# Performance work log

Hardware: AMD Instinct MI355X
Metric: run time of the kernel (lower is better)

## Reference

```python
import jax, jax.numpy as jnp
import numpy as np

EPS = 1e-5

def layer_norm(x, g, b):
    mu = jnp.mean(x, axis=-1, keepdims=True)
    var = jnp.mean(jnp.square(x - mu), axis=-1, keepdims=True)
    return (x - mu) * jax.lax.rsqrt(var + EPS) * g + b

def setup_inputs() -> dict:
    key = jax.random.key(0)
    ks = jax.random.split(key, 8)
    B, T, D, H = 8, 2048, 32, 4
    hd = D // H
    s = 0.05
    return {
        "x": jax.random.normal(ks[0], (B, T, D), jnp.float32),
        "Wq": jax.random.normal(ks[1], (H, D, hd), jnp.float32) * s,
        "Wk": jax.random.normal(ks[2], (H, D, hd), jnp.float32) * s,
        "Wv": jax.random.normal(ks[3], (H, D, hd), jnp.float32) * s,
        "Wproj": jax.random.normal(ks[4], (D, D), jnp.float32) * s,
        "bproj": jnp.zeros((D,), jnp.float32),
        "ln1_g": jnp.ones((D,), jnp.float32),
        "ln1_b": jnp.zeros((D,), jnp.float32),
        "W1": jax.random.normal(ks[5], (D, 4 * D), jnp.float32) * s,
        "b1": jnp.zeros((4 * D,), jnp.float32),
        "W2": jax.random.normal(ks[6], (4 * D, D), jnp.float32) * s,
        "b2": jnp.zeros((D,), jnp.float32),
        "ln2_g": jnp.ones((D,), jnp.float32),
        "ln2_b": jnp.zeros((D,), jnp.float32),
    }

def reference(x, Wq, Wk, Wv, Wproj, bproj, ln1_g, ln1_b, W1, b1, W2, b2, ln2_g, ln2_b):
    B, T, D = x.shape
    H, _, hd = Wq.shape
    scale = hd ** -0.5
    # NOTE: original block normalizes first, and the residual uses the NORMALIZED x
    h = layer_norm(x, ln1_g, ln1_b)                      # (B,T,D)
    q = jnp.einsum('btd,hdk->bhtk', h, Wq)
    k = jnp.einsum('btd,hdk->bhtk', h, Wk)
    v = jnp.einsum('btd,hdk->bhtk', h, Wv)
    scores = jnp.einsum('bhtk,bhsk->bhts', q, k) * scale  # (B,H,T,T)
    mask = jnp.tril(jnp.ones((T, T), bool))
    scores = jnp.where(mask, scores, -jnp.inf)
    attn = jax.nn.softmax(scores, axis=-1)               # dropout = identity (eval)
    o = jnp.einsum('bhts,bhsk->bhtk', attn, v)           # (B,H,T,hd)
    o = o.transpose(0, 2, 1, 3).reshape(B, T, D)         # concat heads, head0 first
    x1 = h + o @ Wproj + bproj
    h2 = layer_norm(x1, ln2_g, ln2_b)
    ff = jax.nn.relu(h2 @ W1 + b1) @ W2 + b2             # dropout = identity (eval)
    return h2 + ff
```

## Files before the change

kernel.cpp:

```cpp
#include <hip/hip_runtime.h>
#include <math.h>

#define BB 8
#define TT 2048
#define DD 32
#define HH 4
#define HD 8
#define NROWS (BB*TT)
#define LNEPS 1e-5f

#if __has_builtin(__builtin_amdgcn_exp2f)
#define EXP2F(x) __builtin_amdgcn_exp2f(x)
#else
#define EXP2F(x) __expf(0.6931471805599453f*(x))
#endif

typedef _Float16 h2 __attribute__((ext_vector_type(2)));
typedef _Float16 h4v __attribute__((ext_vector_type(4)));
typedef _Float16 h8v __attribute__((ext_vector_type(8)));
typedef float f32x16 __attribute__((ext_vector_type(16)));
struct KH { h2 a, b, c, d; };
union F4H { float4 f; KH k; };

static __device__ __forceinline__ h2 pkrtz(float a, float b) {
    return __builtin_bit_cast(h2, __builtin_amdgcn_cvt_pkrtz(a, b));
}
static __device__ __forceinline__ unsigned pkrtz_u(float a, float b) {
    return __builtin_bit_cast(unsigned, __builtin_amdgcn_cvt_pkrtz(a, b));
}
static __device__ __forceinline__ unsigned short f16u(float x) {
    return __builtin_bit_cast(unsigned short, (_Float16)x);
}

#if __has_builtin(__builtin_amdgcn_fdot2)
#define DOT2(a,b,c) __builtin_amdgcn_fdot2((a),(b),(c),false)
#else
#define DOT2(a,b,c) fmaf((float)(a)[1],(float)(b)[1], fmaf((float)(a)[0],(float)(b)[0],(c)))
#endif

__global__ __launch_bounds__(256) void k_ln_qkv(
    const float* __restrict__ x,
    const float* __restrict__ Wq, const float* __restrict__ Wk, const float* __restrict__ Wv,
    const float* __restrict__ g, const float* __restrict__ b,
    float* __restrict__ h, float* __restrict__ qh,
    float* __restrict__ Kh, float* __restrict__ Vt)
{
    __shared__ float sW[3*HH*264];
    __shared__ float sg[DD], sb[DD];
    for (int i = threadIdx.x; i < HH*DD*HD; i += 256) {
        int hd_ = i >> 8, off = i & 255;
        sW[hd_*264 + off]              = Wq[i];
        sW[(4+hd_)*264 + off]          = Wk[i];
        sW[(8+hd_)*264 + off]          = Wv[i];
    }
    if (threadIdx.x < DD) { sg[threadIdx.x] = g[threadIdx.x]; sb[threadIdx.x] = b[threadIdx.x]; }
    __syncthreads();

    int idx = blockIdx.x * 256 + threadIdx.x;
    int r   = idx >> 3;
    int sub = idx & 7;
    int hh  = sub & 3;
    int dh  = sub >> 2;
    int bb  = r >> 11, tt = r & 2047;

    float xr[16];
    {
        const float4* xp = (const float4*)(x + (size_t)r * DD + dh*16);
        float4 t0 = xp[0], t1 = xp[1], t2 = xp[2], t3 = xp[3];
        xr[0]=t0.x; xr[1]=t0.y; xr[2]=t0.z; xr[3]=t0.w;
        xr[4]=t1.x; xr[5]=t1.y; xr[6]=t1.z; xr[7]=t1.w;
        xr[8]=t2.x; xr[9]=t2.y; xr[10]=t2.z; xr[11]=t2.w;
        xr[12]=t3.x; xr[13]=t3.y; xr[14]=t3.z; xr[15]=t3.w;
    }
    float s1 = 0.f;
    #pragma unroll
    for (int i = 0; i < 16; ++i) s1 += xr[i];
    s1 += __shfl_xor(s1, 4, 64);
    float mu = s1 * (1.f/DD);
    float sq = 0.f;
    #pragma unroll
    for (int i = 0; i < 16; ++i) { float d = xr[i]-mu; sq += d*d; }
    sq += __shfl_xor(sq, 4, 64);
    float rs = rsqrtf(sq * (1.f/DD) + LNEPS);

    float hr[16];
    #pragma unroll
    for (int i = 0; i < 16; ++i) hr[i] = (xr[i]-mu)*rs*sg[dh*16+i] + sb[dh*16+i];

    {
        float4* hp = (float4*)(h + (size_t)r * DD + dh*16);
        hp[0]=make_float4(hr[0],hr[1],hr[2],hr[3]);
        hp[1]=make_float4(hr[4],hr[5],hr[6],hr[7]);
        hp[2]=make_float4(hr[8],hr[9],hr[10],hr[11]);
        hp[3]=make_float4(hr[12],hr[13],hr[14],hr[15]);
    }

    const float* wq = sW + hh*264 + dh*128;
    const float* wk = sW + (4+hh)*264 + dh*128;
    const float* wv = sW + (8+hh)*264 + dh*128;
    float qa[HD], ka[HD], va[HD];
    #pragma unroll
    for (int k2 = 0; k2 < HD; ++k2) { qa[k2]=0.f; ka[k2]=0.f; va[k2]=0.f; }
    #pragma unroll
    for (int d = 0; d < 16; ++d) {
        float hv = hr[d];
        const float4* wq4 = (const float4*)(wq + d*8);
        const float4* wk4 = (const float4*)(wk + d*8);
        const float4* wv4 = (const float4*)(wv + d*8);
        float4 a0 = wq4[0], a1 = wq4[1];
        float4 b0 = wk4[0], b1 = wk4[1];
        float4 c0 = wv4[0], c1 = wv4[1];
        qa[0]=fmaf(hv,a0.x,qa[0]); qa[1]=fmaf(hv,a0.y,qa[1]); qa[2]=fmaf(hv,a0.z,qa[2]); qa[3]=fmaf(hv,a0.w,qa[3]);
        qa[4]=fmaf(hv,a1.x,qa[4]); qa[5]=fmaf(hv,a1.y,qa[5]); qa[6]=fmaf(hv,a1.z,qa[6]); qa[7]=fmaf(hv,a1.w,qa[7]);
        ka[0]=fmaf(hv,b0.x,ka[0]); ka[1]=fmaf(hv,b0.y,ka[1]); ka[2]=fmaf(hv,b0.z,ka[2]); ka[3]=fmaf(hv,b0.w,ka[3]);
        ka[4]=fmaf(hv,b1.x,ka[4]); ka[5]=fmaf(hv,b1.y,ka[5]); ka[6]=fmaf(hv,b1.z,ka[6]); ka[7]=fmaf(hv,b1.w,ka[7]);
        va[0]=fmaf(hv,c0.x,va[0]); va[1]=fmaf(hv,c0.y,va[1]); va[2]=fmaf(hv,c0.z,va[2]); va[3]=fmaf(hv,c0.w,va[3]);
        va[4]=fmaf(hv,c1.x,va[4]); va[5]=fmaf(hv,c1.y,va[5]); va[6]=fmaf(hv,c1.z,va[6]); va[7]=fmaf(hv,c1.w,va[7]);
    }
    #pragma unroll
    for (int k2 = 0; k2 < HD; ++k2) {
        qa[k2] += __shfl_xor(qa[k2], 4, 64);
        ka[k2] += __shfl_xor(ka[k2], 4, 64);
        va[k2] += __shfl_xor(va[k2], 4, 64);
    }

    const float SCL = 0.35355339059327373f * 1.4426950408889634f;
    size_t key = (size_t)(bb*HH + hh)*TT + tt;
    char* Vb8 = (char*)Vt + (size_t)(bb*HH + hh)*32768;
    int t6 = tt >> 6, tr = (tt & 63) << 1;
    char* vrow = Vb8 + t6*128;
    if (dh == 0) {
        F4H u;
        u.k.a = pkrtz(qa[0]*SCL, qa[1]*SCL);
        u.k.b = pkrtz(qa[2]*SCL, qa[3]*SCL);
        u.k.c = pkrtz(qa[4]*SCL, qa[5]*SCL);
        u.k.d = pkrtz(qa[6]*SCL, qa[7]*SCL);
        *(float4*)(qh + key*4) = u.f;
        *(unsigned short*)(vrow + 0*4096 + (tr ^ 0))   = f16u(va[0]);
        *(unsigned short*)(vrow + 1*4096 + (tr ^ 16))  = f16u(va[1]);
        *(unsigned short*)(vrow + 2*4096 + (tr ^ 32))  = f16u(va[2]);
        *(unsigned short*)(vrow + 3*4096 + (tr ^ 48))  = f16u(va[3]);
    } else {
        char* Kb8 = (char*)Kh + (size_t)(bb*HH + hh)*32768;
        uint2 k01; k01.x = pkrtz_u(ka[0],ka[1]); k01.y = pkrtz_u(ka[2],ka[3]);
        uint2 k23; k23.x = pkrtz_u(ka[4],ka[5]); k23.y = pkrtz_u(ka[6],ka[7]);
        *(uint2*)(Kb8 + (size_t)tt*8) = k01;
        *(uint2*)(Kb8 + 16384 + (size_t)tt*8) = k23;
        *(unsigned short*)(vrow + 4*4096 + (tr ^ 64))  = f16u(va[4]);
        *(unsigned short*)(vrow + 5*4096 + (tr ^ 80))  = f16u(va[5]);
        *(unsigned short*)(vrow + 6*4096 + (tr ^ 96))  = f16u(va[6]);
        *(unsigned short*)(vrow + 7*4096 + (tr ^ 112)) = f16u(va[7]);
    }
}

template<bool DIAG>
__device__ __forceinline__ void do_chunk(
    const char* __restrict__ smK, const char* __restrict__ smV,
    int kc, int hi, int col, h4v qf,
    float& m, float& l, f32x16& acc)
{
    uint2 kraw = *(const uint2*)(smK + hi*512 + (size_t)(kc + col)*8);
    h4v kf = __builtin_bit_cast(h4v, kraw);
    f32x16 cin;
    #pragma unroll
    for (int r2 = 0; r2 < 16; ++r2) cin[r2] = -m;
    f32x16 S = __builtin_amdgcn_mfma_f32_32x32x8f16(kf, qf, cin, 0, 0, 0);
    if (DIAG) {
        #pragma unroll
        for (int r2 = 0; r2 < 16; ++r2) {
            int row = (r2&3) + 8*(r2>>2) + 4*hi;
            if (row > col) S[r2] = -1e30f;
        }
    }
    float pm = S[0];
    #pragma unroll
    for (int r2 = 1; r2 < 16; ++r2) pm = fmaxf(pm, S[r2]);
    pm = fmaxf(pm, __shfl_xor(pm, 32, 64));
    if (__builtin_expect(__any(pm > 8.f), 0)) {
        float adj = fmaxf(pm, 0.f);
        float cr  = EXP2F(-adj);
        l *= cr;
        #pragma unroll
        for (int r2 = 0; r2 < 16; ++r2) {
            int row = (r2&3) + 8*(r2>>2) + 4*hi;
            acc[r2] *= __shfl(cr, row, 64);
        }
        #pragma unroll
        for (int r2 = 0; r2 < 16; ++r2) S[r2] -= adj;
        m += adj;
    }
    float p[16];
    #pragma unroll
    for (int r2 = 0; r2 < 16; ++r2) p[r2] = EXP2F(S[r2]);
    unsigned pa_ = pkrtz_u(p[0],  p[1]);
    unsigned pb_ = pkrtz_u(p[2],  p[3]);
    unsigned pc_ = pkrtz_u(p[4],  p[5]);
    unsigned pd_ = pkrtz_u(p[6],  p[7]);
    unsigned pe_ = pkrtz_u(p[8],  p[9]);
    unsigned pf_ = pkrtz_u(p[10], p[11]);
    unsigned pg_ = pkrtz_u(p[12], p[13]);
    unsigned ph_ = pkrtz_u(p[14], p[15]);
    const h2 one2 = {(_Float16)1.f, (_Float16)1.f};
    l = DOT2(__builtin_bit_cast(h2, pa_), one2, l);
    l = DOT2(__builtin_bit_cast(h2, pb_), one2, l);
    l = DOT2(__builtin_bit_cast(h2, pc_), one2, l);
    l = DOT2(__builtin_bit_cast(h2, pd_), one2, l);
    l = DOT2(__builtin_bit_cast(h2, pe_), one2, l);
    l = DOT2(__builtin_bit_cast(h2, pf_), one2, l);
    l = DOT2(__builtin_bit_cast(h2, pg_), one2, l);
    l = DOT2(__builtin_bit_cast(h2, ph_), one2, l);
    unsigned ra = (unsigned)__shfl_xor((int)pa_, 32, 64);
    unsigned rb = (unsigned)__shfl_xor((int)pb_, 32, 64);
    unsigned rc = (unsigned)__shfl_xor((int)pc_, 32, 64);
    unsigned rd = (unsigned)__shfl_xor((int)pd_, 32, 64);
    unsigned re = (unsigned)__shfl_xor((int)pe_, 32, 64);
    unsigned rf = (unsigned)__shfl_xor((int)pf_, 32, 64);
    unsigned rg = (unsigned)__shfl_xor((int)pg_, 32, 64);
    unsigned rh = (unsigned)__shfl_xor((int)ph_, 32, 64);
    bool H = (hi != 0);
    uint4 A0 = { H?rc:pa_, H?rd:pb_, H?pc_:ra, H?pd_:rb };
    uint4 A1 = { H?rg:pe_, H?rh:pf_, H?pg_:re, H?ph_:rf };
    int d7 = col & 7;
    const char* vrow = smV + d7*128;
    uint4 v0 = *(const uint4*)(vrow + ((((kc + hi*8) << 1)) ^ (d7 << 4)));
    uint4 v1 = *(const uint4*)(vrow + ((((kc + 16 + hi*8) << 1)) ^ (d7 << 4)));
    acc = __builtin_amdgcn_mfma_f32_32x32x16_f16(
        __builtin_bit_cast(h8v, A0), __builtin_bit_cast(h8v, v0), acc, 0, 0, 0);
    acc = __builtin_amdgcn_mfma_f32_32x32x16_f16(
        __builtin_bit_cast(h8v, A1), __builtin_bit_cast(h8v, v1), acc, 0, 0, 0);
}

__global__ __launch_bounds__(256) void k_attn(
    const float* __restrict__ qh, const float* __restrict__ Kh,
    const float* __restrict__ Vt, float* __restrict__ o)
{
    __shared__ char lds[7168];
    const int tid  = threadIdx.x;
    const int wave = tid >> 6;
    const int lane = tid & 63;
    const int hi   = lane >> 5;
    const int col  = lane & 31;
    const int qg   = wave >> 1;
    const int kh   = wave & 1;
    const int bh   = blockIdx.x & 31;
    const int qblk = 31 - (int)(blockIdx.x >> 5);
    const int qb   = qblk << 6;
    const int wq0  = qb + (qg << 5);
    const int ntiles = qblk + 1;

    const char* Kg = (const char*)Kh + (size_t)bh * 32768;
    const char* Vg = (const char*)Vt + (size_t)bh * 32768;
    const char* Qg = (const char*)qh + (size_t)bh * 32768 + (size_t)wq0 * 16;

    h4v qf = __builtin_bit_cast(h4v, *(const uint2*)(Qg + col*16 + hi*8));

    f32x16 acc;
    #pragma unroll
    for (int r2 = 0; r2 < 16; ++r2) acc[r2] = 0.f;
    float m = 0.f, l = 0.f;

    {
        uint4 st;
        if (tid < 64)       st = *(const uint4*)(Kg + (tid>>5)*16384 + (size_t)(tid&31)*16);
        else if (tid < 128) { int ix = tid-64; st = *(const uint4*)(Vg + (ix>>3)*4096 + (ix&7)*16); }
        if (tid < 64)       *(uint4*)(&lds[0] + (tid>>5)*512 + (tid&31)*16) = st;
        else if (tid < 128) *(uint4*)(&lds[0] + 1024 + (tid-64)*16) = st;
    }
    __syncthreads();

    int buf = 0;
    for (int t = 0; t < ntiles; ++t) {
        uint4 nx;
        const bool more = (t + 1 < ntiles);
        if (more) {
            if (tid < 64)       nx = *(const uint4*)(Kg + (tid>>5)*16384 + (t+1)*512 + (tid&31)*16);
            else if (tid < 128) { int ix = tid-64; nx = *(const uint4*)(Vg + (ix>>3)*4096 + (t+1)*128 + (ix&7)*16); }
        }
        if ((t & 1) == kh) {
            const int tb = t << 6;
            const char* smK = &lds[buf*2048];
            const char* smV = smK + 1024;
            if (tb <= wq0) {
                if (tb == wq0) do_chunk<true >(smK, smV, 0, hi, col, qf, m, l, acc);
                else           do_chunk<false>(smK, smV, 0, hi, col, qf, m, l, acc);
                if (tb + 32 <= wq0) {
                    if (tb + 32 == wq0) do_chunk<true >(smK, smV, 32, hi, col, qf, m, l, acc);
                    else                do_chunk<false>(smK, smV, 32, hi, col, qf, m, l, acc);
                }
            }
        }
        if (more) {
            if (tid < 64)       *(uint4*)(&lds[(buf^1)*2048] + (tid>>5)*512 + (tid&31)*16) = nx;
            else if (tid < 128) *(uint4*)(&lds[(buf^1)*2048] + 1024 + (tid-64)*16) = nx;
        }
        __syncthreads();
        buf ^= 1;
    }

    l += __shfl_xor(l, 32, 64);
    float* mb = (float*)&lds[4096];
    float* lb = (float*)&lds[4608];
    float* ob = (float*)&lds[5120];
    if (lane < 32) {
        mb[(kh<<6) + (qg<<5) + col] = m;
        lb[(kh<<6) + (qg<<5) + col] = l;
    }
    __syncthreads();
    float mo = mb[((kh^1)<<6) + (qg<<5) + col];
    float lo = lb[((kh^1)<<6) + (qg<<5) + col];
    float M  = fmaxf(m, mo);
    float fs = EXP2F(m - M);
    float L  = l * fs + lo * EXP2F(mo - M);
    float Linv = 1.f / L;
    float fr[16], Lr[16];
    #pragma unroll
    for (int r2 = 0; r2 < 16; ++r2) {
        int row = (r2&3) + 8*(r2>>2) + 4*hi;
        fr[r2] = __shfl(fs,   row, 64);
        Lr[r2] = __shfl(Linv, row, 64);
    }
    if (kh == 1 && col < HD) {
        #pragma unroll
        for (int r2 = 0; r2 < 16; ++r2) {
            int row = (r2&3) + 8*(r2>>2) + 4*hi;
            ob[(qg<<8) + (row<<3) + col] = acc[r2] * fr[r2];
        }
    }
    __syncthreads();
    if (kh == 0 && col < HD) {
        float* og = o + ((size_t)bh*TT + wq0)*HD + col;
        #pragma unroll
        for (int r2 = 0; r2 < 16; ++r2) {
            int row = (r2&3) + 8*(r2>>2) + 4*hi;
            og[(size_t)row * HD] = (acc[r2]*fr[r2] + ob[(qg<<8) + (row<<3) + col]) * Lr[r2];
        }
    }
}

__global__ __launch_bounds__(256) void k_proj_ffn(
    const float* __restrict__ h, const float* __restrict__ o,
    const float* __restrict__ Wproj, const float* __restrict__ bproj,
    const float* __restrict__ W1, const float* __restrict__ b1,
    const float* __restrict__ W2, const float* __restrict__ b2,
    const float* __restrict__ g2, const float* __restrict__ bt2,
    float* __restrict__ out)
{
    __shared__ float sWp[DD*36], sW1T[4*DD*36], sW2[4*DD*36];
    __shared__ float sbp[DD], sb1[4*DD], sb2[DD], sg2[DD], sbt2[DD];
    for (int i = threadIdx.x; i < DD*DD; i += 256)      sWp [(i>>5)*36 + (i&31)] = Wproj[i];
    for (int i = threadIdx.x; i < DD*4*DD; i += 256) {
        sW1T[(i&127)*36 + (i>>7)] = W1[i];
        sW2 [(i>>5)*36 + (i&31)]  = W2[i];
    }
    if (threadIdx.x < DD) {
        sbp[threadIdx.x]  = bproj[threadIdx.x];
        sb2[threadIdx.x]  = b2[threadIdx.x];
        sg2[threadIdx.x]  = g2[threadIdx.x];
        sbt2[threadIdx.x] = bt2[threadIdx.x];
    }
    if (threadIdx.x < 4*DD) sb1[threadIdx.x] = b1[threadIdx.x];
    __syncthreads();

    int idx = blockIdx.x * 256 + threadIdx.x;
    int r   = idx >> 3;
    int sub = idx & 7;
    int bb  = r >> 11, tt = r & 2047;

    float o4[4];
    #pragma unroll
    for (int mm = 0; mm < 4; ++mm)
        o4[mm] = o[((size_t)(bb*HH + mm)*TT + tt) * HD + sub];

    float x1[DD];
    #pragma unroll
    for (int d = 0; d < DD; ++d) x1[d] = 0.f;
    #pragma unroll
    for (int mm = 0; mm < 4; ++mm) {
        const float4* wr = (const float4*)&sWp[(sub + 8*mm)*36];
        float ov = o4[mm];
        #pragma unroll
        for (int dc = 0; dc < 8; ++dc) {
            float4 w4 = wr[dc];
            x1[4*dc]   = fmaf(ov, w4.x, x1[4*dc]);
            x1[4*dc+1] = fmaf(ov, w4.y, x1[4*dc+1]);
            x1[4*dc+2] = fmaf(ov, w4.z, x1[4*dc+2]);
            x1[4*dc+3] = fmaf(ov, w4.w, x1[4*dc+3]);
        }
    }
    #pragma unroll
    for (int d = 0; d < DD; ++d) {
        x1[d] += __shfl_xor(x1[d], 1, 64);
        x1[d] += __shfl_xor(x1[d], 2, 64);
        x1[d] += __shfl_xor(x1[d], 4, 64);
    }
    {
        const float4* hp = (const float4*)(h + (size_t)r * DD);
        #pragma unroll
        for (int dc = 0; dc < 8; ++dc) {
            float4 h4 = hp[dc];
            x1[4*dc]   += h4.x + sbp[4*dc];
            x1[4*dc+1] += h4.y + sbp[4*dc+1];
            x1[4*dc+2] += h4.z + sbp[4*dc+2];
            x1[4*dc+3] += h4.w + sbp[4*dc+3];
        }
    }
    float mu = 0.f;
    #pragma unroll
    for (int d = 0; d < DD; ++d) mu += x1[d];
    mu *= (1.f/DD);
    float var = 0.f;
    #pragma unroll
    for (int d = 0; d < DD; ++d) { float dl = x1[d]-mu; var += dl*dl; }
    var *= (1.f/DD);
    float rs = rsqrtf(var + LNEPS);
    float h2v[DD];
    #pragma unroll
    for (int d = 0; d < DD; ++d) h2v[d] = (x1[d]-mu)*rs*sg2[d] + sbt2[d];

    float outp[DD];
    #pragma unroll
    for (int d = 0; d < DD; ++d) outp[d] = 0.f;
    #pragma unroll
    for (int mm = 0; mm < 16; ++mm) {
        int j = sub + 8*mm;
        const float4* w1r = (const float4*)&sW1T[j*36];
        float a = sb1[j];
        #pragma unroll
        for (int dc = 0; dc < 8; ++dc) {
            float4 w4 = w1r[dc];
            a = fmaf(h2v[4*dc], w4.x, a);
            a = fmaf(h2v[4*dc+1], w4.y, a);
            a = fmaf(h2v[4*dc+2], w4.z, a);
            a = fmaf(h2v[4*dc+3], w4.w, a);
        }
        a = fmaxf(a, 0.f);
        const float4* w2r = (const float4*)&sW2[j*36];
        #pragma unroll
        for (int dc = 0; dc < 8; ++dc) {
            float4 w4 = w2r[dc];
            outp[4*dc]   = fmaf(a, w4.x, outp[4*dc]);
            outp[4*dc+1] = fmaf(a, w4.y, outp[4*dc+1]);
            outp[4*dc+2] = fmaf(a, w4.z, outp[4*dc+2]);
            outp[4*dc+3] = fmaf(a, w4.w, outp[4*dc+3]);
        }
    }
    if (sub == 0) {
        #pragma unroll
        for (int d = 0; d < DD; ++d) outp[d] += h2v[d] + sb2[d];
    }
    float t1[16];
    #pragma unroll
    for (int i = 0; i < 16; ++i) {
        bool hib = (sub & 4) != 0;
        float send = hib ? outp[i] : outp[i+16];
        float recv = __shfl_xor(send, 4, 64);
        t1[i] = (hib ? outp[i+16] : outp[i]) + recv;
    }
    float t2[8];
    #pragma unroll
    for (int i = 0; i < 8; ++i) {
        bool hib = (sub & 2) != 0;
        float send = hib ? t1[i] : t1[i+8];
        float recv = __shfl_xor(send, 2, 64);
        t2[i] = (hib ? t1[i+8] : t1[i]) + recv;
    }
    float w0[4];
    #pragma unroll
    for (int i = 0; i < 4; ++i) {
        bool hib = (sub & 1) != 0;
        float send = hib ? t2[i] : t2[i+4];
        float recv = __shfl_xor(send, 1, 64);
        w0[i] = (hib ? t2[i+4] : t2[i]) + recv;
    }
    *(float4*)(out + (size_t)r * DD + sub*4) = make_float4(w0[0], w0[1], w0[2], w0[3]);
}

extern "C" void kernel_launch(void* const* d_in, const int* in_sizes, int n_in,
                              void* d_out, int out_size, void* d_ws, size_t ws_size,
                              hipStream_t stream) {
    const float* x     = (const float*)d_in[0];
    const float* Wq    = (const float*)d_in[1];
    const float* Wk    = (const float*)d_in[2];
    const float* Wv    = (const float*)d_in[3];
    const float* Wproj = (const float*)d_in[4];
    const float* bproj = (const float*)d_in[5];
    const float* ln1_g = (const float*)d_in[6];
    const float* ln1_b = (const float*)d_in[7];
    const float* W1    = (const float*)d_in[8];
    const float* b1    = (const float*)d_in[9];
    const float* W2    = (const float*)d_in[10];
    const float* b2    = (const float*)d_in[11];
    const float* ln2_g = (const float*)d_in[12];
    const float* ln2_b = (const float*)d_in[13];
    float* out = (float*)d_out;

    const size_t N = (size_t)NROWS * DD;
    const size_t K = (size_t)BB*HH*TT*4;
    float* ws = (float*)d_ws;
    float* h  = ws;
    float* qh = ws + N;
    float* Kh = ws + N + K;
    float* Vt = ws + N + 2*K;
    float* o  = ws + N + 3*K;

    k_ln_qkv  <<<512, 256, 0, stream>>>(x, Wq, Wk, Wv, ln1_g, ln1_b, h, qh, Kh, Vt);
    k_attn    <<<1024, 256, 0, stream>>>(qh, Kh, Vt, o);
    k_proj_ffn<<<512, 256, 0, stream>>>(h, o, Wproj, bproj, W1, b1, W2, b2, ln2_g, ln2_b, out);
}
```

Measured before the change: 137.7 us.

## Load K/V straight from global into registers, drop LDS tiling and block barriers

The attention kernel stops staging K/V tiles through double-buffered LDS with a __syncthreads per tile. Each wave now loads its 32-key chunk of K and V directly from global memory into registers, with software prefetch of the next chunk. The V layout written by the QKV kernel changes from a swizzled 64-key tile format to a plain transposed layout to match. Work is remapped so each block handles two independent 32-row query tiles, split across wave pairs that process alternating key chunks. This removes the per-tile barrier and LDS traffic, at the cost of redundant global and L2 reads across waves and less load coalescing.

```diff
diff --git a/kernel.cpp b/kernel.cpp
--- a/kernel.cpp
+++ b/kernel.cpp
@@ -126,9 +126,7 @@
 
     const float SCL = 0.35355339059327373f * 1.4426950408889634f;
     size_t key = (size_t)(bb*HH + hh)*TT + tt;
-    char* Vb8 = (char*)Vt + (size_t)(bb*HH + hh)*32768;
-    int t6 = tt >> 6, tr = (tt & 63) << 1;
-    char* vrow = Vb8 + t6*128;
+    unsigned short* vtb = (unsigned short*)Vt + (size_t)(bb*HH + hh)*8*TT + tt;
     if (dh == 0) {
         F4H u;
         u.k.a = pkrtz(qa[0]*SCL, qa[1]*SCL);
@@ -136,30 +134,28 @@
         u.k.c = pkrtz(qa[4]*SCL, qa[5]*SCL);
         u.k.d = pkrtz(qa[6]*SCL, qa[7]*SCL);
         *(float4*)(qh + key*4) = u.f;
-        *(unsigned short*)(vrow + 0*4096 + (tr ^ 0))   = f16u(va[0]);
-        *(unsigned short*)(vrow + 1*4096 + (tr ^ 16))  = f16u(va[1]);
-        *(unsigned short*)(vrow + 2*4096 + (tr ^ 32))  = f16u(va[2]);
-        *(unsigned short*)(vrow + 3*4096 + (tr ^ 48))  = f16u(va[3]);
+        vtb[(size_t)0*TT] = f16u(va[0]);
+        vtb[(size_t)1*TT] = f16u(va[1]);
+        vtb[(size_t)2*TT] = f16u(va[2]);
+        vtb[(size_t)3*TT] = f16u(va[3]);
     } else {
         char* Kb8 = (char*)Kh + (size_t)(bb*HH + hh)*32768;
         uint2 k01; k01.x = pkrtz_u(ka[0],ka[1]); k01.y = pkrtz_u(ka[2],ka[3]);
         uint2 k23; k23.x = pkrtz_u(ka[4],ka[5]); k23.y = pkrtz_u(ka[6],ka[7]);
         *(uint2*)(Kb8 + (size_t)tt*8) = k01;
         *(uint2*)(Kb8 + 16384 + (size_t)tt*8) = k23;
-        *(unsigned short*)(vrow + 4*4096 + (tr ^ 64))  = f16u(va[4]);
-        *(unsigned short*)(vrow + 5*4096 + (tr ^ 80))  = f16u(va[5]);
-        *(unsigned short*)(vrow + 6*4096 + (tr ^ 96))  = f16u(va[6]);
-        *(unsigned short*)(vrow + 7*4096 + (tr ^ 112)) = f16u(va[7]);
+        vtb[(size_t)4*TT] = f16u(va[4]);
+        vtb[(size_t)5*TT] = f16u(va[5]);
+        vtb[(size_t)6*TT] = f16u(va[6]);
+        vtb[(size_t)7*TT] = f16u(va[7]);
     }
 }
 
 template<bool DIAG>
-__device__ __forceinline__ void do_chunk(
-    const char* __restrict__ smK, const char* __restrict__ smV,
-    int kc, int hi, int col, h4v qf,
-    float& m, float& l, f32x16& acc)
+__device__ __forceinline__ void chunk_compute(
+    uint2 kraw, uint4 v0r, uint4 v1r, int hi, int col,
+    h4v qf, float& m, float& l, f32x16& acc)
 {
-    uint2 kraw = *(const uint2*)(smK + hi*512 + (size_t)(kc + col)*8);
     h4v kf = __builtin_bit_cast(h4v, kraw);
     f32x16 cin;
     #pragma unroll
@@ -220,37 +216,35 @@
     bool H = (hi != 0);
     uint4 A0 = { H?rc:pa_, H?rd:pb_, H?pc_:ra, H?pd_:rb };
     uint4 A1 = { H?rg:pe_, H?rh:pf_, H?pg_:re, H?ph_:rf };
-    int d7 = col & 7;
-    const char* vrow = smV + d7*128;
-    uint4 v0 = *(const uint4*)(vrow + ((((kc + hi*8) << 1)) ^ (d7 << 4)));
-    uint4 v1 = *(const uint4*)(vrow + ((((kc + 16 + hi*8) << 1)) ^ (d7 << 4)));
     acc = __builtin_amdgcn_mfma_f32_32x32x16_f16(
-        __builtin_bit_cast(h8v, A0), __builtin_bit_cast(h8v, v0), acc, 0, 0, 0);
+        __builtin_bit_cast(h8v, A0), __builtin_bit_cast(h8v, v0r), acc, 0, 0, 0);
     acc = __builtin_amdgcn_mfma_f32_32x32x16_f16(
-        __builtin_bit_cast(h8v, A1), __builtin_bit_cast(h8v, v1), acc, 0, 0, 0);
+        __builtin_bit_cast(h8v, A1), __builtin_bit_cast(h8v, v1r), acc, 0, 0, 0);
 }
 
 __global__ __launch_bounds__(256) void k_attn(
     const float* __restrict__ qh, const float* __restrict__ Kh,
     const float* __restrict__ Vt, float* __restrict__ o)
 {
-    __shared__ char lds[7168];
+    __shared__ float mb[128];
+    __shared__ float lb[128];
+    __shared__ float ob[512];
     const int tid  = threadIdx.x;
     const int wave = tid >> 6;
     const int lane = tid & 63;
     const int hi   = lane >> 5;
     const int col  = lane & 31;
-    const int qg   = wave >> 1;
-    const int kh   = wave & 1;
-    const int bh   = blockIdx.x & 31;
-    const int qblk = 31 - (int)(blockIdx.x >> 5);
-    const int qb   = qblk << 6;
-    const int wq0  = qb + (qg << 5);
-    const int ntiles = qblk + 1;
+    const int tl   = wave >> 1;
+    const int p    = wave & 1;
+    const int T    = blockIdx.x * 2 + tl;
+    const int qi   = 63 - (T >> 5);
+    const int bh   = T & 31;
+    const int wq0  = qi << 5;
 
     const char* Kg = (const char*)Kh + (size_t)bh * 32768;
     const char* Vg = (const char*)Vt + (size_t)bh * 32768;
     const char* Qg = (const char*)qh + (size_t)bh * 32768 + (size_t)wq0 * 16;
+    const char* vrow = Vg + (size_t)(col & 7) * 4096;
 
     h4v qf = __builtin_bit_cast(h4v, *(const uint2*)(Qg + col*16 + hi*8));
 
@@ -259,55 +253,37 @@
     for (int r2 = 0; r2 < 16; ++r2) acc[r2] = 0.f;
     float m = 0.f, l = 0.f;
 
-    {
-        uint4 st;
-        if (tid < 64)       st = *(const uint4*)(Kg + (tid>>5)*16384 + (size_t)(tid&31)*16);
-        else if (tid < 128) { int ix = tid-64; st = *(const uint4*)(Vg + (ix>>3)*4096 + (ix&7)*16); }
-        if (tid < 64)       *(uint4*)(&lds[0] + (tid>>5)*512 + (tid&31)*16) = st;
-        else if (tid < 128) *(uint4*)(&lds[0] + 1024 + (tid-64)*16) = st;
+#define LOADC(c, K2, V0, V1) do { \
+    K2 = *(const uint2*)(Kg + hi*16384 + (size_t)((((c)<<5) + col))*8); \
+    V0 = *(const uint4*)(vrow + (size_t)((((c)<<5) + (hi<<3)))*2); \
+    V1 = *(const uint4*)(vrow + (size_t)((((c)<<5) + 16 + (hi<<3)))*2); \
+} while (0)
+
+    const int last = ((qi & 1) == p) ? qi : qi - 1;
+    if (last >= p) {
+        uint2 kc_; uint4 v0c, v1c;
+        LOADC(p, kc_, v0c, v1c);
+        int c = p;
+        while (c < last) {
+            uint2 kn_; uint4 v0n, v1n;
+            LOADC(c + 2, kn_, v0n, v1n);
+            chunk_compute<false>(kc_, v0c, v1c, hi, col, qf, m, l, acc);
+            kc_ = kn_; v0c = v0n; v1c = v1n;
+            c += 2;
+        }
+        if (last == qi) chunk_compute<true >(kc_, v0c, v1c, hi, col, qf, m, l, acc);
+        else            chunk_compute<false>(kc_, v0c, v1c, hi, col, qf, m, l, acc);
+    }
+#undef LOADC
+
+    l += __shfl_xor(l, 32, 64);
+    if (lane < 32) {
+        mb[tl*64 + p*32 + col] = m;
+        lb[tl*64 + p*32 + col] = l;
     }
     __syncthreads();
-
-    int buf = 0;
-    for (int t = 0; t < ntiles; ++t) {
-        uint4 nx;
-        const bool more = (t + 1 < ntiles);
-        if (more) {
-            if (tid < 64)       nx = *(const uint4*)(Kg + (tid>>5)*16384 + (t+1)*512 + (tid&31)*16);
-            else if (tid < 128) { int ix = tid-64; nx = *(const uint4*)(Vg + (ix>>3)*4096 + (t+1)*128 + (ix&7)*16); }
-        }
-        if ((t & 1) == kh) {
-            const int tb = t << 6;
-            const char* smK = &lds[buf*2048];
-            const char* smV = smK + 1024;
-            if (tb <= wq0) {
-                if (tb == wq0) do_chunk<true >(smK, smV, 0, hi, col, qf, m, l, acc);
-                else           do_chunk<false>(smK, smV, 0, hi, col, qf, m, l, acc);
-                if (tb + 32 <= wq0) {
-                    if (tb + 32 == wq0) do_chunk<true >(smK, smV, 32, hi, col, qf, m, l, acc);
-                    else                do_chunk<false>(smK, smV, 32, hi, col, qf, m, l, acc);
-                }
-            }
-        }
-        if (more) {
-            if (tid < 64)       *(uint4*)(&lds[(buf^1)*2048] + (tid>>5)*512 + (tid&31)*16) = nx;
-            else if (tid < 128) *(uint4*)(&lds[(buf^1)*2048] + 1024 + (tid-64)*16) = nx;
-        }
-        __syncthreads();
-        buf ^= 1;
-    }
-
-    l += __shfl_xor(l, 32, 64);
-    float* mb = (float*)&lds[4096];
-    float* lb = (float*)&lds[4608];
-    float* ob = (float*)&lds[5120];
-    if (lane < 32) {
-        mb[(kh<<6) + (qg<<5) + col] = m;
-        lb[(kh<<6) + (qg<<5) + col] = l;
-    }
-    __syncthreads();
-    float mo = mb[((kh^1)<<6) + (qg<<5) + col];
-    float lo = lb[((kh^1)<<6) + (qg<<5) + col];
+    float mo = mb[tl*64 + (p^1)*32 + col];
+    float lo = lb[tl*64 + (p^1)*32 + col];
     float M  = fmaxf(m, mo);
     float fs = EXP2F(m - M);
     float L  = l * fs + lo * EXP2F(mo - M);
@@ -319,20 +295,20 @@
         fr[r2] = __shfl(fs,   row, 64);
         Lr[r2] = __shfl(Linv, row, 64);
     }
-    if (kh == 1 && col < HD) {
+    if (p == 1 && col < HD) {
         #pragma unroll
         for (int r2 = 0; r2 < 16; ++r2) {
             int row = (r2&3) + 8*(r2>>2) + 4*hi;
-            ob[(qg<<8) + (row<<3) + col] = acc[r2] * fr[r2];
+            ob[tl*256 + (row<<3) + col] = acc[r2] * fr[r2];
         }
     }
     __syncthreads();
-    if (kh == 0 && col < HD) {
+    if (p == 0 && col < HD) {
         float* og = o + ((size_t)bh*TT + wq0)*HD + col;
         #pragma unroll
         for (int r2 = 0; r2 < 16; ++r2) {
             int row = (r2&3) + 8*(r2>>2) + 4*hi;
-            og[(size_t)row * HD] = (acc[r2]*fr[r2] + ob[(qg<<8) + (row<<3) + col]) * Lr[r2];
+            og[(size_t)row * HD] = (acc[r2]*fr[r2] + ob[tl*256 + (row<<3) + col]) * Lr[r2];
         }
     }
 }
```

Measured after the change: 123.0 us (median of 2 runs). -10.6%, faster.
